# Kernel tuning notes

Measured on AMD Instinct MI355X. Metric: run time of the kernel, lower is better.

Reference implementation:

```python
import jax, jax.numpy as jnp
import numpy as np

N = 100000      # nodes
E = 1600000     # directed edges (made undirected in reference)
G = 256         # graphs in batch
DIN, H, DOUT, C = 192, 64, 32, 2


def setup_inputs() -> dict:
    key = jax.random.key(0)
    ks = jax.random.split(key, 12)
    x = jax.random.normal(ks[0], (N, DIN), jnp.float32)
    src = jax.random.randint(ks[1], (E,), 0, N, dtype=jnp.int32)
    off = jax.random.randint(ks[2], (E,), 1, N, dtype=jnp.int32)
    dst = (src + off) % N  # avoids self-loops; duplicates statistically negligible
    edge_index = jnp.stack([src, dst]).astype(jnp.int32)
    batch = jnp.sort(jax.random.randint(ks[3], (N,), 0, G, dtype=jnp.int32))
    s = lambda d: 1.0 / np.sqrt(d)
    W_in = jax.random.normal(ks[4], (DIN, H), jnp.float32) * s(DIN)
    b_in = jnp.zeros((H,), jnp.float32)
    W1 = jax.random.normal(ks[5], (H, H), jnp.float32) * s(H)
    b1 = jnp.zeros((H,), jnp.float32)
    W2 = jax.random.normal(ks[6], (H, H), jnp.float32) * s(H)
    b2 = jnp.zeros((H,), jnp.float32)
    Wf1 = jax.random.normal(ks[7], (H, DOUT), jnp.float32) * s(H)
    bf1 = jnp.zeros((DOUT,), jnp.float32)
    Wf2 = jax.random.normal(ks[8], (DOUT, C), jnp.float32) * s(DOUT)
    bf2 = jnp.zeros((C,), jnp.float32)
    return dict(x=x, edge_index=edge_index, batch=batch, num_graphs=G,
                W_in=W_in, b_in=b_in, W1=W1, b1=b1, W2=W2, b2=b2,
                Wf1=Wf1, bf1=bf1, Wf2=Wf2, bf2=bf2)


def _gcn_conv(x, src, dst, deg_inv_sqrt, W, b):
    # x' = D^{-1/2}(A + I)D^{-1/2} X W + b  (GCNConv w/ self-loops, default norm)
    h = x @ W                                            # [N,H]
    coef = deg_inv_sqrt[src] * deg_inv_sqrt[dst]         # [E2]
    msg = h[src] * coef[:, None]                         # gather + scale
    agg = jax.ops.segment_sum(msg, dst, num_segments=x.shape[0])
    agg = agg + h * (deg_inv_sqrt * deg_inv_sqrt)[:, None]  # self-loop term
    return agg + b


def reference(x, edge_index, batch, num_graphs, W_in, b_in, W1, b1, W2, b2,
              Wf1, bf1, Wf2, bf2):
    # to_undirected: both directions (input assumed duplicate-free)
    src = jnp.concatenate([edge_index[0], edge_index[1]])
    dst = jnp.concatenate([edge_index[1], edge_index[0]])
    n = x.shape[0]
    # degree with self-loop (+1), symmetric since edges are bidirectional
    deg = jax.ops.segment_sum(jnp.ones_like(dst, jnp.float32), dst,
                              num_segments=n) + 1.0
    dis = jax.lax.rsqrt(deg)

    h = jax.nn.relu(x @ W_in + b_in)
    h = jax.nn.relu(_gcn_conv(h, src, dst, dis, W1, b1))
    h = jax.nn.relu(_gcn_conv(h, src, dst, dis, W2, b2))

    # global_mean_pool over batch ids
    sums = jax.ops.segment_sum(h, batch, num_segments=num_graphs)
    cnt = jax.ops.segment_sum(jnp.ones((n,), jnp.float32), batch,
                              num_segments=num_graphs)
    pooled = sums / jnp.maximum(cnt, 1.0)[:, None]

    out = jax.nn.relu(pooled @ Wf1 + bf1) @ Wf2 + bf2
    return jax.nn.log_softmax(out, axis=1)
```

## Files before the change

### kernel.cpp

```cpp
#include <hip/hip_runtime.h>
#include <hip/hip_bf16.h>
#include <hip/hip_fp16.h>

#define NMAX   100000
#define EMAX   1600000
#define NGRAPH 256
#define DIN    192
#define HDIM   64
#define DOUTD  32
#define NCLS   2
#define TNI    64
#define XP     68
#define NB_SHIFT 8
#define NBUCK  ((NMAX >> NB_SHIFT) + 1)
#define T1E    2048
#define P2CAP  15872

typedef float f2v __attribute__((ext_vector_type(2)));

__device__ float         g_dis[NMAX];
__device__ float         g_h[NMAX * HDIM];
__device__ unsigned char g_t8[NMAX * HDIM];
__device__ int           g_row[NMAX + 1];
__device__ int           g_col[2 * EMAX];
__device__ unsigned      g_stage[2 * EMAX];
__device__ int           g_bcnt[NBUCK];
__device__ int           g_bbase[NBUCK + 1];
__device__ int           g_bcur[NBUCK];
__device__ int           g_gptr[NGRAPH + 1];
__device__ int           g_cc;
__device__ int           g_flag;

__device__ __forceinline__ void load_edge(const int* __restrict__ ei, int E, int e,
                                          int& s, int& d) {
    if (g_flag) { s = ei[2 * e]; d = ei[2 * e + 1]; }
    else        { s = ei[e];     d = ei[e + E];     }
}

__global__ __launch_bounds__(256) void k_count(const int* __restrict__ ei, int E) {
    __shared__ int hcnt[NBUCK];
    for (int b = threadIdx.x; b < NBUCK; b += 256) hcnt[b] = 0;
    __syncthreads();
    int stride = gridDim.x * 256;
    for (int e = blockIdx.x * 256 + threadIdx.x; e < E; e += stride) {
        int a = ei[e];
        int c = ei[e + E];
        if (a == c) atomicAdd(&g_cc, 1);
        atomicAdd(&hcnt[a >> NB_SHIFT], 1);
        atomicAdd(&hcnt[c >> NB_SHIFT], 1);
    }
    __syncthreads();
    for (int b = threadIdx.x; b < NBUCK; b += 256) {
        int v = hcnt[b];
        if (v) atomicAdd(&g_bcnt[b], v);
    }
}

__global__ __launch_bounds__(512) void k_meta(const int* __restrict__ batch, int n) {
    __shared__ int sh[512];
    int tid = threadIdx.x;
    if (blockIdx.x == 0) {
        int c = (tid < NBUCK) ? g_bcnt[tid] : 0;
        sh[tid] = c;
        __syncthreads();
        for (int off = 1; off < 512; off <<= 1) {
            int t = (tid >= off) ? sh[tid - off] : 0;
            __syncthreads();
            sh[tid] += t;
            __syncthreads();
        }
        if (tid < NBUCK) {
            int base = sh[tid] - c;
            g_bbase[tid] = base;
            g_bcur[tid]  = base;
            g_bcnt[tid]  = 0;
        }
        if (tid == NBUCK - 1) g_bbase[NBUCK] = sh[tid];
        if (tid == 0) { g_flag = (g_cc != 0) ? 1 : 0; g_cc = 0; }
    } else {
        int i = (blockIdx.x - 1) * 512 + tid;
        if (i > n) return;
        if (i == 0) {
            int b0 = batch[0];
            for (int g = 0; g <= b0; ++g) g_gptr[g] = 0;
        } else if (i == n) {
            int bl = batch[n - 1];
            for (int g = bl + 1; g <= NGRAPH; ++g) g_gptr[g] = n;
        } else {
            int bp = batch[i - 1], bc = batch[i];
            for (int g = bp + 1; g <= bc; ++g) g_gptr[g] = i;
        }
    }
}

__global__ __launch_bounds__(512) void k_stage(const int* __restrict__ ei, int E) {
    __shared__ int2 sbuf[2 * T1E];
    __shared__ int  scnt[NBUCK], soff[NBUCK], sput[NBUCK], sbase[NBUCK];
    __shared__ int  sc[512];
    int tid = threadIdx.x;
    int e0  = blockIdx.x * T1E;
    for (int b = tid; b < NBUCK; b += 512) { scnt[b] = 0; sput[b] = 0; }
    __syncthreads();

    int s[4], d[4];
    #pragma unroll
    for (int it = 0; it < 4; ++it) {
        int e = e0 + it * 512 + tid;
        if (e < E) {
            load_edge(ei, E, e, s[it], d[it]);
            atomicAdd(&scnt[d[it] >> NB_SHIFT], 1);
            atomicAdd(&scnt[s[it] >> NB_SHIFT], 1);
        } else s[it] = -1;
    }
    __syncthreads();

    sc[tid] = (tid < NBUCK) ? scnt[tid] : 0;
    __syncthreads();
    for (int off = 1; off < 512; off <<= 1) {
        int t = (tid >= off) ? sc[tid - off] : 0;
        __syncthreads();
        sc[tid] += t;
        __syncthreads();
    }
    for (int b = tid; b < NBUCK; b += 512) {
        soff[b] = sc[b] - scnt[b];
        if (scnt[b] > 0) sbase[b] = atomicAdd(&g_bcur[b], scnt[b]);
    }
    __syncthreads();

    #pragma unroll
    for (int it = 0; it < 4; ++it) {
        if (s[it] >= 0) {
            int bd = d[it] >> NB_SHIFT;
            sbuf[soff[bd] + atomicAdd(&sput[bd], 1)] = make_int2(d[it], s[it]);
            int bs = s[it] >> NB_SHIFT;
            sbuf[soff[bs] + atomicAdd(&sput[bs], 1)] = make_int2(s[it], d[it]);
        }
    }
    __syncthreads();

    int total = sc[NBUCK - 1];
    for (int i = tid; i < total; i += 512) {
        int2 pr = sbuf[i];
        int  b  = pr.x >> NB_SHIFT;
        unsigned packed = ((unsigned)(pr.x & 255) << 24) | (unsigned)pr.y;
        g_stage[sbase[b] + (i - soff[b])] = packed;
    }
}

__global__ __launch_bounds__(512) void k_scatter(int n) {
    __shared__ int cols[P2CAP];
    __shared__ int cur[256];
    int b  = blockIdx.x;
    int v0 = b << NB_SHIFT;
    if (v0 >= n) return;
    int v1   = min(v0 + 256, n);
    int base = g_bbase[b];
    int len  = g_bbase[b + 1] - base;
    int tid  = threadIdx.x;

    if (tid < 256) cur[tid] = 0;
    __syncthreads();
    for (int i = tid; i < len; i += 512) {
        unsigned p = g_stage[base + i];
        atomicAdd(&cur[p >> 24], 1);
    }
    __syncthreads();

    int d = (tid < 256) ? cur[tid] : 0;
    for (int off = 1; off < 256; off <<= 1) {
        int t = (tid < 256 && tid >= off) ? cur[tid - off] : 0;
        __syncthreads();
        if (tid < 256) cur[tid] += t;
        __syncthreads();
    }
    if (tid < 256) {
        int excl = cur[tid] - d;
        if (v0 + tid < v1) {
            g_row[v0 + tid] = base + excl;
            g_dis[v0 + tid] = 1.0f / sqrtf((float)d + 1.0f);
        }
    }
    if (tid == 0 && v1 == n) g_row[n] = base + len;
    __syncthreads();
    if (tid < 256) cur[tid] -= d;
    __syncthreads();

    for (int i = tid; i < len; i += 512) {
        unsigned p  = g_stage[base + i];
        int pos = atomicAdd(&cur[p >> 24], 1);
        int val = (int)(p & 0xFFFFFFu);
        if (pos < P2CAP) cols[pos] = val;
        else             g_col[base + pos] = val;
    }
    __syncthreads();
    int lim = len < P2CAP ? len : P2CAP;
    for (int i = tid; i < lim; i += 512)
        g_col[base + i] = cols[i];
}

__device__ __forceinline__ void store_msg(int node, int fg, float dv,
                                          float a0, float a1, float a2, float a3) {
    int w = __builtin_amdgcn_cvt_pk_fp8_f32(dv * a0, dv * a1, 0, false);
    w     = __builtin_amdgcn_cvt_pk_fp8_f32(dv * a2, dv * a3, w, true);
    *(unsigned*)(g_t8 + ((size_t)node << 6) + fg * 4) = (unsigned)w;
}

__device__ __forceinline__ float4 ld_msg4(int node, int f4) {
    unsigned u = *(const unsigned*)(g_t8 + ((size_t)node << 6) + f4 * 4);
    f2v lo = __builtin_amdgcn_cvt_pk_f32_fp8((int)u, false);
    f2v hi = __builtin_amdgcn_cvt_pk_f32_fp8((int)u, true);
    return make_float4(lo.x, lo.y, hi.x, hi.y);
}

__global__ __launch_bounds__(256) void k_inhw(const float* __restrict__ x,
                                              const float* __restrict__ Win,
                                              const float* __restrict__ bin,
                                              const float* __restrict__ W1, int n) {
    __shared__ float sh[TNI][XP];
    __shared__ float sw[64 * HDIM];
    int tid = threadIdx.x;
    int fg  = tid & 15;
    int ng  = tid >> 4;
    int n0  = blockIdx.x * TNI;

    float acc[4][4];
    #pragma unroll
    for (int i = 0; i < 4; ++i)
        #pragma unroll
        for (int j = 0; j < 4; ++j) acc[i][j] = 0.0f;

    for (int c = 0; c < DIN / 64; ++c) {
        int k0 = c * 64;
        __syncthreads();
        #pragma unroll
        for (int p = 0; p < 4; ++p) {
            int row = p * 16 + ng;
            int col = fg * 4;
            float4 v = make_float4(0.f, 0.f, 0.f, 0.f);
            if (n0 + row < n)
                v = *(const float4*)(x + (size_t)(n0 + row) * DIN + k0 + col);
            *(float4*)&sh[row][col] = v;
        }
        {
            const float4* wsrc = (const float4*)(Win + (size_t)k0 * HDIM);
            float4*       wdst = (float4*)sw;
            #pragma unroll
            for (int p = 0; p < 4; ++p) wdst[tid + p * 256] = wsrc[tid + p * 256];
        }
        __syncthreads();
        #pragma unroll 8
        for (int k = 0; k < 64; ++k) {
            float4 w = *(const float4*)&sw[k * HDIM + fg * 4];
            #pragma unroll
            for (int i = 0; i < 4; ++i) {
                float xv = sh[i * 16 + ng][k];
                acc[i][0] += xv * w.x; acc[i][1] += xv * w.y;
                acc[i][2] += xv * w.z; acc[i][3] += xv * w.w;
            }
        }
    }
    __syncthreads();
    {
        const float4* wsrc = (const float4*)W1;
        float4*       wdst = (float4*)sw;
        #pragma unroll
        for (int p = 0; p < 4; ++p) wdst[tid + p * 256] = wsrc[tid + p * 256];
    }
    float4 bb = *(const float4*)(bin + fg * 4);
    #pragma unroll
    for (int i = 0; i < 4; ++i) {
        float4 hv;
        hv.x = fmaxf(acc[i][0] + bb.x, 0.f);
        hv.y = fmaxf(acc[i][1] + bb.y, 0.f);
        hv.z = fmaxf(acc[i][2] + bb.z, 0.f);
        hv.w = fmaxf(acc[i][3] + bb.w, 0.f);
        *(float4*)&sh[i * 16 + ng][fg * 4] = hv;
        acc[i][0] = acc[i][1] = acc[i][2] = acc[i][3] = 0.0f;
    }
    __syncthreads();
    #pragma unroll 8
    for (int k = 0; k < 64; ++k) {
        float4 w = *(const float4*)&sw[k * HDIM + fg * 4];
        #pragma unroll
        for (int i = 0; i < 4; ++i) {
            float hv = sh[i * 16 + ng][k];
            acc[i][0] += hv * w.x; acc[i][1] += hv * w.y;
            acc[i][2] += hv * w.z; acc[i][3] += hv * w.w;
        }
    }
    #pragma unroll
    for (int i = 0; i < 4; ++i) {
        int node = n0 + i * 16 + ng;
        if (node < n)
            store_msg(node, fg, g_dis[node], acc[i][0], acc[i][1], acc[i][2], acc[i][3]);
    }
}

__global__ __launch_bounds__(256) void k_hw2(const float* __restrict__ W2, int n) {
    __shared__ float sh[TNI][XP];
    __shared__ float sw[64 * HDIM];
    int tid = threadIdx.x;
    int fg  = tid & 15;
    int ng  = tid >> 4;
    int n0  = blockIdx.x * TNI;

    #pragma unroll
    for (int p = 0; p < 4; ++p) {
        int row = p * 16 + ng;
        int col = fg * 4;
        float4 v = make_float4(0.f, 0.f, 0.f, 0.f);
        if (n0 + row < n)
            v = *(const float4*)(g_h + (size_t)(n0 + row) * HDIM + col);
        *(float4*)&sh[row][col] = v;
    }
    {
        const float4* wsrc = (const float4*)W2;
        float4*       wdst = (float4*)sw;
        #pragma unroll
        for (int p = 0; p < 4; ++p) wdst[tid + p * 256] = wsrc[tid + p * 256];
    }
    __syncthreads();
    float acc[4][4];
    #pragma unroll
    for (int i = 0; i < 4; ++i)
        #pragma unroll
        for (int j = 0; j < 4; ++j) acc[i][j] = 0.0f;
    #pragma unroll 8
    for (int k = 0; k < 64; ++k) {
        float4 w = *(const float4*)&sw[k * HDIM + fg * 4];
        #pragma unroll
        for (int i = 0; i < 4; ++i) {
            float hv = sh[i * 16 + ng][k];
            acc[i][0] += hv * w.x; acc[i][1] += hv * w.y;
            acc[i][2] += hv * w.z; acc[i][3] += hv * w.w;
        }
    }
    #pragma unroll
    for (int i = 0; i < 4; ++i) {
        int node = n0 + i * 16 + ng;
        if (node < n)
            store_msg(node, fg, g_dis[node], acc[i][0], acc[i][1], acc[i][2], acc[i][3]);
    }
}

__global__ void k_gather(const float* __restrict__ b, int n) {
    int v = (blockIdx.x * blockDim.x + threadIdx.x) >> 6;
    if (v >= n) return;
    int lane = threadIdx.x & 63;
    int f4   = lane & 15;
    int sub  = lane >> 4;
    int beg = g_row[v], end = g_row[v + 1];
    float4 acc = make_float4(0.f, 0.f, 0.f, 0.f);
    int j = beg;
    for (; j + 16 <= end; j += 16) {
        int a0 = g_col[j + 0 + sub];
        int a1 = g_col[j + 4 + sub];
        int a2 = g_col[j + 8 + sub];
        int a3 = g_col[j + 12 + sub];
        float4 f0 = ld_msg4(a0, f4);
        float4 f1 = ld_msg4(a1, f4);
        float4 f2 = ld_msg4(a2, f4);
        float4 f3 = ld_msg4(a3, f4);
        acc.x += (f0.x + f1.x) + (f2.x + f3.x);
        acc.y += (f0.y + f1.y) + (f2.y + f3.y);
        acc.z += (f0.z + f1.z) + (f2.z + f3.z);
        acc.w += (f0.w + f1.w) + (f2.w + f3.w);
    }
    if (j + 8 <= end) {
        int a0 = g_col[j + 0 + sub];
        int a1 = g_col[j + 4 + sub];
        float4 f0 = ld_msg4(a0, f4);
        float4 f1 = ld_msg4(a1, f4);
        acc.x += f0.x + f1.x;
        acc.y += f0.y + f1.y;
        acc.z += f0.z + f1.z;
        acc.w += f0.w + f1.w;
        j += 8;
    }
    if (j + 4 <= end) {
        int a0 = g_col[j + sub];
        float4 f0 = ld_msg4(a0, f4);
        acc.x += f0.x; acc.y += f0.y; acc.z += f0.z; acc.w += f0.w;
        j += 4;
    }
    int r = end - j;
    if (sub < r) {
        int u = g_col[j + sub];
        float4 f0 = ld_msg4(u, f4);
        acc.x += f0.x; acc.y += f0.y; acc.z += f0.z; acc.w += f0.w;
    }
    acc.x += __shfl_xor(acc.x, 16, 64); acc.y += __shfl_xor(acc.y, 16, 64);
    acc.z += __shfl_xor(acc.z, 16, 64); acc.w += __shfl_xor(acc.w, 16, 64);
    acc.x += __shfl_xor(acc.x, 32, 64); acc.y += __shfl_xor(acc.y, 32, 64);
    acc.z += __shfl_xor(acc.z, 32, 64); acc.w += __shfl_xor(acc.w, 32, 64);
    if (sub == 0) {
        float4 sf = ld_msg4(v, f4);
        float dv  = g_dis[v];
        float4 bb = *((const float4*)b + f4);
        float4 o;
        o.x = fmaxf(dv * (acc.x + sf.x) + bb.x, 0.f);
        o.y = fmaxf(dv * (acc.y + sf.y) + bb.y, 0.f);
        o.z = fmaxf(dv * (acc.z + sf.z) + bb.z, 0.f);
        o.w = fmaxf(dv * (acc.w + sf.w) + bb.w, 0.f);
        *((float4*)(g_h + (size_t)v * HDIM) + f4) = o;
    }
}

__global__ void k_poolhead(const float* __restrict__ Wf1, const float* __restrict__ bf1,
                           const float* __restrict__ Wf2, const float* __restrict__ bf2,
                           float* __restrict__ out) {
    __shared__ float ps[4][HDIM];
    __shared__ float p[HDIM];
    __shared__ float z[DOUTD];
    int g   = blockIdx.x;
    int tid = threadIdx.x;
    int f   = tid & 63, q = tid >> 6;
    int beg = g_gptr[g], end = g_gptr[g + 1];
    float s = 0.0f;
    for (int i = beg + q; i < end; i += 4)
        s += __builtin_nontemporal_load(&g_h[(size_t)i * HDIM + f]);
    ps[q][f] = s;
    __syncthreads();
    if (tid < HDIM) {
        float cnt = fmaxf((float)(end - beg), 1.0f);
        p[tid] = (ps[0][tid] + ps[1][tid] + ps[2][tid] + ps[3][tid]) / cnt;
    }
    __syncthreads();
    if (tid < DOUTD) {
        float a = bf1[tid];
        for (int k = 0; k < HDIM; ++k)
            a += p[k] * Wf1[k * DOUTD + tid];
        z[tid] = fmaxf(a, 0.0f);
    }
    __syncthreads();
    if (tid == 0) {
        float l0 = bf2[0], l1 = bf2[1];
        for (int k = 0; k < DOUTD; ++k) {
            l0 += z[k] * Wf2[k * NCLS + 0];
            l1 += z[k] * Wf2[k * NCLS + 1];
        }
        float m   = fmaxf(l0, l1);
        float lse = m + logf(expf(l0 - m) + expf(l1 - m));
        out[g * NCLS + 0] = l0 - lse;
        out[g * NCLS + 1] = l1 - lse;
    }
}

extern "C" void kernel_launch(void* const* d_in, const int* in_sizes, int n_in,
                              void* d_out, int out_size, void* d_ws, size_t ws_size,
                              hipStream_t stream) {
    (void)d_ws; (void)ws_size; (void)out_size;

    const float* x   = (const float*)d_in[0];
    const int*   ei  = (const int*)d_in[1];
    const int*   bat = (const int*)d_in[2];

    const float* wp[10] = {nullptr};
    int wi = 0;
    for (int i = 3; i < n_in && wi < 10; ++i) {
        if (in_sizes[i] == 1) continue;
        wp[wi++] = (const float*)d_in[i];
    }
    const float* W_in = wp[0];
    const float* b_in = wp[1];
    const float* W1   = wp[2];
    const float* b1   = wp[3];
    const float* W2   = wp[4];
    const float* b2   = wp[5];
    const float* Wf1  = wp[6];
    const float* bf1  = wp[7];
    const float* Wf2  = wp[8];
    const float* bf2  = wp[9];

    const int n = in_sizes[0] / DIN;
    const int E = in_sizes[1] / 2;

    const int B = 256;
    int gNH    = (int)(((long long)n * HDIM + B - 1) / B);
    int gTile  = (n + TNI - 1) / TNI;
    int gStage = (E + T1E - 1) / T1E;
    int gMeta  = 1 + (n + 1 + 511) / 512;

    k_count<<<512, 256, 0, stream>>>(ei, E);
    k_meta<<<gMeta, 512, 0, stream>>>(bat, n);

    k_stage<<<gStage, 512, 0, stream>>>(ei, E);
    k_scatter<<<NBUCK, 512, 0, stream>>>(n);

    k_inhw<<<gTile, 256, 0, stream>>>(x, W_in, b_in, W1, n);
    k_gather<<<gNH, B, 0, stream>>>(b1, n);

    k_hw2<<<gTile, 256, 0, stream>>>(W2, n);
    k_gather<<<gNH, B, 0, stream>>>(b2, n);

    k_poolhead<<<NGRAPH, 256, 0, stream>>>(Wf1, bf1, Wf2, bf2, (float*)d_out);
}
```

Measured before the change: 391.8 us.

## Use fp16 MFMA for dense input and hidden-layer projections

```diff
diff --git a/kernel.cpp b/kernel.cpp
--- a/kernel.cpp
+++ b/kernel.cpp
@@ -10,13 +10,15 @@
 #define DOUTD  32
 #define NCLS   2
 #define TNI    64
-#define XP     68
+#define FP     72
 #define NB_SHIFT 8
 #define NBUCK  ((NMAX >> NB_SHIFT) + 1)
 #define T1E    2048
 #define P2CAP  15872
 
-typedef float f2v __attribute__((ext_vector_type(2)));
+typedef float    f2v  __attribute__((ext_vector_type(2)));
+typedef float    f32x4 __attribute__((ext_vector_type(4)));
+typedef _Float16 h4   __attribute__((ext_vector_type(4)));
 
 __device__ float         g_dis[NMAX];
 __device__ float         g_h[NMAX * HDIM];
@@ -199,11 +201,9 @@
         g_col[base + i] = cols[i];
 }
 
-__device__ __forceinline__ void store_msg(int node, int fg, float dv,
-                                          float a0, float a1, float a2, float a3) {
-    int w = __builtin_amdgcn_cvt_pk_fp8_f32(dv * a0, dv * a1, 0, false);
-    w     = __builtin_amdgcn_cvt_pk_fp8_f32(dv * a2, dv * a3, w, true);
-    *(unsigned*)(g_t8 + ((size_t)node << 6) + fg * 4) = (unsigned)w;
+__device__ __forceinline__ unsigned char enc_fp8(float v) {
+    int w = __builtin_amdgcn_cvt_pk_fp8_f32(v, v, 0, false);
+    return (unsigned char)(w & 0xff);
 }
 
 __device__ __forceinline__ float4 ld_msg4(int node, int f4) {
@@ -213,134 +213,151 @@
     return make_float4(lo.x, lo.y, hi.x, hi.y);
 }
 
+__device__ __forceinline__ void mfma_strip(const _Float16 (*xh)[FP],
+                                           const _Float16 (*wt)[FP],
+                                           int wv, int lane, int klen,
+                                           f32x4 acc[4]) {
+    int r16 = lane & 15;
+    int kg  = (lane >> 4) * 4;
+    for (int k0 = 0; k0 < klen; k0 += 16) {
+        h4 a = *(const h4*)&xh[wv * 16 + r16][k0 + kg];
+        #pragma unroll
+        for (int nt = 0; nt < 4; ++nt) {
+            h4 b = *(const h4*)&wt[nt * 16 + r16][k0 + kg];
+            acc[nt] = __builtin_amdgcn_mfma_f32_16x16x16f16(a, b, acc[nt], 0, 0, 0);
+        }
+    }
+}
+
 __global__ __launch_bounds__(256) void k_inhw(const float* __restrict__ x,
                                               const float* __restrict__ Win,
                                               const float* __restrict__ bin,
                                               const float* __restrict__ W1, int n) {
-    __shared__ float sh[TNI][XP];
-    __shared__ float sw[64 * HDIM];
-    int tid = threadIdx.x;
-    int fg  = tid & 15;
-    int ng  = tid >> 4;
-    int n0  = blockIdx.x * TNI;
-
-    float acc[4][4];
-    #pragma unroll
-    for (int i = 0; i < 4; ++i)
-        #pragma unroll
-        for (int j = 0; j < 4; ++j) acc[i][j] = 0.0f;
+    __shared__ _Float16 xh[TNI][FP];
+    __shared__ _Float16 wt[TNI][FP];
+    int tid  = threadIdx.x;
+    int lane = tid & 63;
+    int wv   = tid >> 6;
+    int n0   = blockIdx.x * TNI;
+
+    f32x4 acc[4];
+    #pragma unroll
+    for (int nt = 0; nt < 4; ++nt) acc[nt] = (f32x4)0.0f;
 
     for (int c = 0; c < DIN / 64; ++c) {
         int k0 = c * 64;
         __syncthreads();
         #pragma unroll
         for (int p = 0; p < 4; ++p) {
-            int row = p * 16 + ng;
-            int col = fg * 4;
+            int u   = p * 256 + tid;
+            int row = u >> 4;
+            int c4  = u & 15;
             float4 v = make_float4(0.f, 0.f, 0.f, 0.f);
             if (n0 + row < n)
-                v = *(const float4*)(x + (size_t)(n0 + row) * DIN + k0 + col);
-            *(float4*)&sh[row][col] = v;
-        }
-        {
-            const float4* wsrc = (const float4*)(Win + (size_t)k0 * HDIM);
-            float4*       wdst = (float4*)sw;
-            #pragma unroll
-            for (int p = 0; p < 4; ++p) wdst[tid + p * 256] = wsrc[tid + p * 256];
-        }
-        __syncthreads();
-        #pragma unroll 8
-        for (int k = 0; k < 64; ++k) {
-            float4 w = *(const float4*)&sw[k * HDIM + fg * 4];
+                v = *(const float4*)(x + (size_t)(n0 + row) * DIN + k0 + c4 * 4);
+            h4 hv = { (_Float16)v.x, (_Float16)v.y, (_Float16)v.z, (_Float16)v.w };
+            *(h4*)&xh[row][c4 * 4] = hv;
+        }
+        #pragma unroll
+        for (int p = 0; p < 16; ++p) {
+            int u  = p * 256 + tid;
+            int kk = u >> 6;
+            int nn = u & 63;
+            wt[nn][kk] = (_Float16)Win[(size_t)(k0 + kk) * HDIM + nn];
+        }
+        __syncthreads();
+        mfma_strip(xh, wt, wv, lane, 64, acc);
+    }
+
+    __syncthreads();
+    {
+        int rg = (lane >> 4) * 4;
+        #pragma unroll
+        for (int nt = 0; nt < 4; ++nt) {
+            int col = nt * 16 + (lane & 15);
+            float bb = bin[col];
             #pragma unroll
             for (int i = 0; i < 4; ++i) {
-                float xv = sh[i * 16 + ng][k];
-                acc[i][0] += xv * w.x; acc[i][1] += xv * w.y;
-                acc[i][2] += xv * w.z; acc[i][3] += xv * w.w;
+                float hv = fmaxf(acc[nt][i] + bb, 0.f);
+                xh[wv * 16 + rg + i][col] = (_Float16)hv;
             }
-        }
-    }
-    __syncthreads();
+            acc[nt] = (f32x4)0.0f;
+        }
+    }
+    #pragma unroll
+    for (int p = 0; p < 16; ++p) {
+        int u  = p * 256 + tid;
+        int kk = u >> 6;
+        int nn = u & 63;
+        wt[nn][kk] = (_Float16)W1[(size_t)kk * HDIM + nn];
+    }
+    __syncthreads();
+    mfma_strip(xh, wt, wv, lane, 64, acc);
+
     {
-        const float4* wsrc = (const float4*)W1;
-        float4*       wdst = (float4*)sw;
-        #pragma unroll
-        for (int p = 0; p < 4; ++p) wdst[tid + p * 256] = wsrc[tid + p * 256];
-    }
-    float4 bb = *(const float4*)(bin + fg * 4);
-    #pragma unroll
-    for (int i = 0; i < 4; ++i) {
-        float4 hv;
-        hv.x = fmaxf(acc[i][0] + bb.x, 0.f);
-        hv.y = fmaxf(acc[i][1] + bb.y, 0.f);
-        hv.z = fmaxf(acc[i][2] + bb.z, 0.f);
-        hv.w = fmaxf(acc[i][3] + bb.w, 0.f);
-        *(float4*)&sh[i * 16 + ng][fg * 4] = hv;
-        acc[i][0] = acc[i][1] = acc[i][2] = acc[i][3] = 0.0f;
-    }
-    __syncthreads();
-    #pragma unroll 8
-    for (int k = 0; k < 64; ++k) {
-        float4 w = *(const float4*)&sw[k * HDIM + fg * 4];
+        int rg = (lane >> 4) * 4;
         #pragma unroll
         for (int i = 0; i < 4; ++i) {
-            float hv = sh[i * 16 + ng][k];
-            acc[i][0] += hv * w.x; acc[i][1] += hv * w.y;
-            acc[i][2] += hv * w.z; acc[i][3] += hv * w.w;
-        }
-    }
-    #pragma unroll
-    for (int i = 0; i < 4; ++i) {
-        int node = n0 + i * 16 + ng;
-        if (node < n)
-            store_msg(node, fg, g_dis[node], acc[i][0], acc[i][1], acc[i][2], acc[i][3]);
+            int node = n0 + wv * 16 + rg + i;
+            if (node < n) {
+                float dv = g_dis[node];
+                #pragma unroll
+                for (int nt = 0; nt < 4; ++nt) {
+                    int col = nt * 16 + (lane & 15);
+                    g_t8[((size_t)node << 6) + col] = enc_fp8(dv * acc[nt][i]);
+                }
+            }
+        }
     }
 }
 
 __global__ __launch_bounds__(256) void k_hw2(const float* __restrict__ W2, int n) {
-    __shared__ float sh[TNI][XP];
-    __shared__ float sw[64 * HDIM];
-    int tid = threadIdx.x;
-    int fg  = tid & 15;
-    int ng  = tid >> 4;
-    int n0  = blockIdx.x * TNI;
+    __shared__ _Float16 xh[TNI][FP];
+    __shared__ _Float16 wt[TNI][FP];
+    int tid  = threadIdx.x;
+    int lane = tid & 63;
+    int wv   = tid >> 6;
+    int n0   = blockIdx.x * TNI;
 
     #pragma unroll
     for (int p = 0; p < 4; ++p) {
-        int row = p * 16 + ng;
-        int col = fg * 4;
+        int u   = p * 256 + tid;
+        int row = u >> 4;
+        int c4  = u & 15;
         float4 v = make_float4(0.f, 0.f, 0.f, 0.f);
         if (n0 + row < n)
-            v = *(const float4*)(g_h + (size_t)(n0 + row) * HDIM + col);
-        *(float4*)&sh[row][col] = v;
-    }
+            v = *(const float4*)(g_h + (size_t)(n0 + row) * HDIM + c4 * 4);
+        h4 hv = { (_Float16)v.x, (_Float16)v.y, (_Float16)v.z, (_Float16)v.w };
+        *(h4*)&xh[row][c4 * 4] = hv;
+    }
+    #pragma unroll
+    for (int p = 0; p < 16; ++p) {
+        int u  = p * 256 + tid;
+        int kk = u >> 6;
+        int nn = u & 63;
+        wt[nn][kk] = (_Float16)W2[(size_t)kk * HDIM + nn];
+    }
+    __syncthreads();
+
+    f32x4 acc[4];
+    #pragma unroll
+    for (int nt = 0; nt < 4; ++nt) acc[nt] = (f32x4)0.0f;
+    mfma_strip(xh, wt, wv, lane, 64, acc);
+
     {
-        const float4* wsrc = (const float4*)W2;
-        float4*       wdst = (float4*)sw;
-        #pragma unroll
-        for (int p = 0; p < 4; ++p) wdst[tid + p * 256] = wsrc[tid + p * 256];
-    }
-    __syncthreads();
-    float acc[4][4];
-    #pragma unroll
-    for (int i = 0; i < 4; ++i)
-        #pragma unroll
-        for (int j = 0; j < 4; ++j) acc[i][j] = 0.0f;
-    #pragma unroll 8
-    for (int k = 0; k < 64; ++k) {
-        float4 w = *(const float4*)&sw[k * HDIM + fg * 4];
+        int rg = (lane >> 4) * 4;
         #pragma unroll
         for (int i = 0; i < 4; ++i) {
-            float hv = sh[i * 16 + ng][k];
-            acc[i][0] += hv * w.x; acc[i][1] += hv * w.y;
-            acc[i][2] += hv * w.z; acc[i][3] += hv * w.w;
-        }
-    }
-    #pragma unroll
-    for (int i = 0; i < 4; ++i) {
-        int node = n0 + i * 16 + ng;
-        if (node < n)
-            store_msg(node, fg, g_dis[node], acc[i][0], acc[i][1], acc[i][2], acc[i][3]);
+            int node = n0 + wv * 16 + rg + i;
+            if (node < n) {
+                float dv = g_dis[node];
+                #pragma unroll
+                for (int nt = 0; nt < 4; ++nt) {
+                    int col = nt * 16 + (lane & 15);
+                    g_t8[((size_t)node << 6) + col] = enc_fp8(dv * acc[nt][i]);
+                }
+            }
+        }
     }
 }
 
```

Result: faster. 373.8 us (-4.6%).
